# Optimization experiments

Hardware: AMD Instinct MI355X
Metric: run time of the kernel (lower is better)

The kernel has to match this reference:

```python
import jax, jax.numpy as jnp
import numpy as np

D_MODEL, D_STATE, D_CONV, EXPAND = 1024, 16, 4, 2
D_INNER = EXPAND * D_MODEL            # 2048
DT_RANK = int(np.ceil(D_MODEL / 16))  # 64
B, L = 2, 2048


def _dt_bias(key):
    # matches torch init: dt ~ exp(U(log dt_min, log dt_max)), inv via softplus inverse
    dt = jnp.exp(jax.random.uniform(key, (D_INNER,)) * (np.log(0.1) - np.log(0.001)) + np.log(0.001))
    dt = jnp.clip(dt, 1e-4, None)
    return dt + jnp.log(-jnp.expm1(-dt))


def _A_log():
    return jnp.log(jnp.tile(jnp.arange(1, D_STATE + 1, dtype=jnp.float32)[None, :], (D_INNER, 1)))


def setup_inputs() -> dict:
    key = jax.random.key(0)
    ks = jax.random.split(key, 16)
    n = lambda k, shape, s=0.02: jax.random.normal(k, shape, jnp.float32) * s
    return {
        "hidden_states": jax.random.normal(ks[0], (B, L, D_MODEL), jnp.float32),
        "in_proj_w": n(ks[1], (2 * D_INNER, D_MODEL)),
        "conv_w": n(ks[2], (D_INNER, 1, D_CONV), 0.2),
        "conv_b": jnp.zeros((D_INNER,), jnp.float32),
        "x_proj_w": n(ks[3], (DT_RANK + 2 * D_STATE, D_INNER)),
        "dt_proj_w": n(ks[4], (D_INNER, DT_RANK), 0.1),
        "dt_proj_b": _dt_bias(ks[5]),
        "A_log": _A_log(),
        "D": jnp.ones((D_INNER,), jnp.float32),
        "conv_w_b": n(ks[6], (D_INNER, 1, D_CONV), 0.2),
        "conv_b_b": jnp.zeros((D_INNER,), jnp.float32),
        "x_proj_w_b": n(ks[7], (DT_RANK + 2 * D_STATE, D_INNER)),
        "dt_proj_w_b": n(ks[8], (D_INNER, DT_RANK), 0.1),
        "dt_proj_b_b": _dt_bias(ks[9]),
        "A_b_log": _A_log(),
        "D_b": jnp.ones((D_INNER,), jnp.float32),
        "out_proj_w": n(ks[10], (D_MODEL, D_INNER)),
    }


def _silu(x):
    return x * jax.nn.sigmoid(x)


def _causal_dw_conv(x, w, b):
    # x: (B, Di, L); w: (Di, 1, K) depthwise; left-pad K-1 => causal, output length L
    y = jax.lax.conv_general_dilated(
        x, w, window_strides=(1,), padding=[(D_CONV - 1, 0)],
        dimension_numbers=("NCH", "OIH", "NCH"), feature_group_count=x.shape[1])
    return y + b[None, :, None]


def _mamba_branch(xz, conv_w, conv_b, x_proj_w, dt_proj_w, dt_proj_b, A_log, Dp):
    # xz: (B, 2*Di, L) -> y: (B, Di, L); selective scan (mamba_inner_fn_no_out_proj)
    x, z = jnp.split(xz, 2, axis=1)
    x = _silu(_causal_dw_conv(x, conv_w, conv_b))                       # (B,Di,L)
    x_dbl = jnp.einsum('rd,bdl->brl', x_proj_w, x)
    dt_r, Bc, Cc = jnp.split(x_dbl, [DT_RANK, DT_RANK + D_STATE], axis=1)
    delta = jax.nn.softplus(jnp.einsum('dr,brl->bdl', dt_proj_w, dt_r) + dt_proj_b[None, :, None])
    A = -jnp.exp(A_log)                                                 # (Di,N)

    def step(h, inp):
        d_t, u_t, b_t, c_t = inp   # (B,Di),(B,Di),(B,N),(B,N)
        h = h * jnp.exp(d_t[..., None] * A) + (d_t * u_t)[..., None] * b_t[:, None, :]
        return h, jnp.einsum('bdn,bn->bd', h, c_t)

    h0 = jnp.zeros((x.shape[0], D_INNER, D_STATE), x.dtype)
    xs = (jnp.moveaxis(delta, 2, 0), jnp.moveaxis(x, 2, 0),
          jnp.moveaxis(Bc, 2, 0), jnp.moveaxis(Cc, 2, 0))
    _, ys = jax.lax.scan(step, h0, xs)                                  # (L,B,Di)
    y = jnp.moveaxis(ys, 0, 2) + x * Dp[None, :, None]
    return y * _silu(z)


def reference(hidden_states, in_proj_w, conv_w, conv_b, x_proj_w, dt_proj_w, dt_proj_b,
              A_log, D, conv_w_b, conv_b_b, x_proj_w_b, dt_proj_w_b, dt_proj_b_b,
              A_b_log, D_b, out_proj_w):
    # bimamba_type == 'v2': forward scan + flipped backward scan, summed, then out_proj (no biases)
    xz = jnp.einsum('ed,bld->bel', in_proj_w, hidden_states)            # (B, 2*Di, L)
    out_f = _mamba_branch(xz, conv_w, conv_b, x_proj_w, dt_proj_w, dt_proj_b, A_log, D)
    out_r = _mamba_branch(xz[..., ::-1], conv_w_b, conv_b_b, x_proj_w_b,
                          dt_proj_w_b, dt_proj_b_b, A_b_log, D_b)[..., ::-1]
    y = out_f + out_r                                                   # (B,Di,L)
    return jnp.einsum('me,bel->blm', out_proj_w, y)                     # (B,L,D)
```

## Files before the change

kernel.cpp:

```cpp
#include <hip/hip_runtime.h>
#include <hip/hip_bf16.h>
#include <math.h>


#define L_SEQ  2048
#define B_SZ   2
#define DM     1024
#define DI     2048
#define NST    16
#define RTOT   96
#define DTR    64
#define NTOT   (B_SZ * L_SEQ)
#define ETOT   (2 * DI)
#define NCH    32
#define CHT    (L_SEQ / NCH)
#define SPLK   8

#define OFF_X    ((size_t)0)
#define OFF_ZT   (OFF_X   + (size_t)DI * NTOT)
#define OFF_XCF  (OFF_ZT  + (size_t)DI * NTOT)
#define OFF_XCB  (OFF_XCF + (size_t)DI * NTOT)
#define OFF_DLTB (OFF_XCB + (size_t)DI * NTOT)
#define OFF_XDF  (OFF_DLTB + (size_t)DI * NTOT)
#define OFF_XDB  (OFF_XDF + (size_t)RTOT * NTOT)
#define OFF_SS   (OFF_XDB + (size_t)RTOT * NTOT)
#define OFF_HL   (OFF_SS  + (size_t)4 * NCH * DI)
#define OFF_YGTF (OFF_HL  + (size_t)4 * NCH * NST * DI)
#define OFF_YGTB (OFF_YGTF + (size_t)NTOT * DI / 2)
#define OFF_XDT16F (OFF_YGTB + (size_t)NTOT * DI / 2)
#define OFF_XDT16B (OFF_XDT16F + (size_t)NTOT * DTR / 2)
#define OFF_DTW16F (OFF_XDT16B + (size_t)NTOT * DTR / 2)
#define OFF_DTW16B (OFF_DTW16F + (size_t)DI * DTR / 2)
#define WS_FLOATS  (OFF_DTW16B + (size_t)DI * DTR / 2)

typedef __bf16 bf16x8 __attribute__((ext_vector_type(8)));
typedef float  floatx4 __attribute__((ext_vector_type(4)));

__device__ __forceinline__ float silu_f(float x) {
    return x / (1.f + __expf(-x));
}

__device__ __forceinline__ void gl2lds16(const __bf16* g, __bf16* l) {
    __builtin_amdgcn_global_load_lds(
        (const __attribute__((address_space(1))) unsigned int*)g,
        (__attribute__((address_space(3))) unsigned int*)l, 16, 0, 0);
}

template<int MT, bool TRANS, bool SPLITZ>
__global__ __launch_bounds__(256)
void gemm_bf16(const __bf16* __restrict__ A, const __bf16* __restrict__ B,
               float* __restrict__ C, float* __restrict__ C2,
               int M, int N, int K)
{
    static_assert(MT == 64 || MT == 128, "vmcnt literals assume MT in {64,128}");
    __shared__ __attribute__((aligned(16))) __bf16 As[2][MT * 32];
    __shared__ __attribute__((aligned(16))) __bf16 Bs[2][128 * 32];
    const int tid  = threadIdx.x;
    const int m0   = blockIdx.y * MT;
    const int n0   = blockIdx.x * 128;
    const int lane = tid & 63;
    const int wave = tid >> 6;
    const int wy   = wave >> 1, wx = wave & 1;
    const int lr   = lane & 15;
    const int q    = lane >> 4;
    constexpr int MF = MT / 32;

    floatx4 acc[MF][4];
#pragma unroll
    for (int i = 0; i < MF; ++i)
#pragma unroll
        for (int j = 0; j < 4; ++j) acc[i][j] = (floatx4)(0.0f);

    const int rl = lane >> 2;
    const int cp = lane & 3;
    const int sw = (q ^ ((lr >> 2) & 3)) * 8;

    auto stage = [&](int s, int k0) {
#pragma unroll
        for (int is = 0; is < MT / 64; ++is) {
            int r0  = wave * (MT / 4) + is * 16;
            int row = r0 + rl;
            int c   = cp ^ ((row >> 2) & 3);
            gl2lds16(A + (size_t)(m0 + row) * K + k0 + c * 8, &As[s][r0 * 32]);
        }
#pragma unroll
        for (int is = 0; is < 2; ++is) {
            int r0  = wave * 32 + is * 16;
            int row = r0 + rl;
            int c   = cp ^ ((row >> 2) & 3);
            gl2lds16(B + (size_t)(n0 + row) * K + k0 + c * 8, &Bs[s][r0 * 32]);
        }
    };

    stage(0, 0);
    int cur = 0;
    for (int k0 = 0; k0 < K; k0 += 32) {
        if (k0 + 32 < K) {
            stage(cur ^ 1, k0 + 32);
            if constexpr (MT == 128) {
                asm volatile("s_waitcnt vmcnt(4)" ::: "memory");
            } else {
                asm volatile("s_waitcnt vmcnt(3)" ::: "memory");
            }
        } else {
            asm volatile("s_waitcnt vmcnt(0)" ::: "memory");
        }
        __builtin_amdgcn_s_barrier();

        bf16x8 af[MF], bfr[4];
#pragma unroll
        for (int i = 0; i < MF; ++i)
            af[i] = *(const bf16x8*)&As[cur][(wy * (MT / 2) + i * 16 + lr) * 32 + sw];
#pragma unroll
        for (int j = 0; j < 4; ++j)
            bfr[j] = *(const bf16x8*)&Bs[cur][(wx * 64 + j * 16 + lr) * 32 + sw];
#pragma unroll
        for (int i = 0; i < MF; ++i)
#pragma unroll
            for (int j = 0; j < 4; ++j)
                acc[i][j] = __builtin_amdgcn_mfma_f32_16x16x32_bf16(
                    af[i], bfr[j], acc[i][j], 0, 0, 0);
        __builtin_amdgcn_s_barrier();
        cur ^= 1;
    }

    const int mb = m0 + wy * (MT / 2);
    const int nb = n0 + wx * 64;
#pragma unroll
    for (int i = 0; i < MF; ++i) {
#pragma unroll
        for (int j = 0; j < 4; ++j) {
            int gn  = nb + j * 16 + lr;
            int gm0 = mb + i * 16 + q * 4;
            if constexpr (SPLITZ) {
                if (m0 < DI) {
#pragma unroll
                    for (int r = 0; r < 4; ++r)
                        C[(size_t)(gm0 + r) * N + gn] = acc[i][j][r];
                } else {
                    *(floatx4*)&C2[(size_t)gn * DI + (gm0 - DI)] = acc[i][j];
                }
            } else if constexpr (TRANS) {
                *(floatx4*)&C[(size_t)gn * M + gm0] = acc[i][j];
            } else {
#pragma unroll
                for (int r = 0; r < 4; ++r)
                    C[(size_t)(gm0 + r) * N + gn] = acc[i][j][r];
            }
        }
    }
}

__global__ __launch_bounds__(256)
void dtproj_mfma(const __bf16* __restrict__ Af, const __bf16* __restrict__ Ab,
                 const __bf16* __restrict__ Bwf, const __bf16* __restrict__ Bwb,
                 const float* __restrict__ bif, const float* __restrict__ bib,
                 float* __restrict__ outf, float* __restrict__ outb)
{
    __shared__ __attribute__((aligned(16))) __bf16 As[2][128 * 32];
    __shared__ __attribute__((aligned(16))) __bf16 Bs[2][128 * 32];
    const int br = blockIdx.z;
    const __bf16* A  = br ? Ab : Af;
    const __bf16* B  = br ? Bwb : Bwf;
    const float*  bi = br ? bib : bif;
    float*        C  = br ? outb : outf;

    const int tid  = threadIdx.x;
    const int m0   = blockIdx.y * 128;
    const int n0   = blockIdx.x * 128;
    const int lane = tid & 63;
    const int wave = tid >> 6;
    const int wy   = wave >> 1, wx = wave & 1;
    const int lr   = lane & 15;
    const int q    = lane >> 4;

    floatx4 acc[4][4];
#pragma unroll
    for (int i = 0; i < 4; ++i)
#pragma unroll
        for (int j = 0; j < 4; ++j) acc[i][j] = (floatx4)(0.0f);

    const int rl = lane >> 2;
    const int cp = lane & 3;
    const int sw = (q ^ ((lr >> 2) & 3)) * 8;

#pragma unroll
    for (int t = 0; t < 2; ++t) {
        int k0 = t * 32;
#pragma unroll
        for (int is = 0; is < 2; ++is) {
            int r0  = wave * 32 + is * 16;
            int row = r0 + rl;
            int c   = cp ^ ((row >> 2) & 3);
            gl2lds16(A + (size_t)(m0 + row) * DTR + k0 + c * 8, &As[t][r0 * 32]);
            gl2lds16(B + (size_t)(n0 + row) * DTR + k0 + c * 8, &Bs[t][r0 * 32]);
        }
    }

#pragma unroll
    for (int t = 0; t < 2; ++t) {
        if (t == 0) asm volatile("s_waitcnt vmcnt(4)" ::: "memory");
        else        asm volatile("s_waitcnt vmcnt(0)" ::: "memory");
        __builtin_amdgcn_s_barrier();

        bf16x8 af[4], bfr[4];
#pragma unroll
        for (int i = 0; i < 4; ++i)
            af[i] = *(const bf16x8*)&As[t][(wy * 64 + i * 16 + lr) * 32 + sw];
#pragma unroll
        for (int j = 0; j < 4; ++j)
            bfr[j] = *(const bf16x8*)&Bs[t][(wx * 64 + j * 16 + lr) * 32 + sw];
#pragma unroll
        for (int i = 0; i < 4; ++i)
#pragma unroll
            for (int j = 0; j < 4; ++j)
                acc[i][j] = __builtin_amdgcn_mfma_f32_16x16x32_bf16(
                    af[i], bfr[j], acc[i][j], 0, 0, 0);
    }

    const int mb = m0 + wy * 64;
    const int nb = n0 + wx * 64;
    float bj[4];
#pragma unroll
    for (int j = 0; j < 4; ++j) bj[j] = bi[nb + j * 16 + lr];
#pragma unroll
    for (int i = 0; i < 4; ++i) {
#pragma unroll
        for (int r = 0; r < 4; ++r) {
            int gm = mb + i * 16 + q * 4 + r;
#pragma unroll
            for (int j = 0; j < 4; ++j) {
                int gn = nb + j * 16 + lr;
                float x = acc[i][j][r] + bj[j];
                float o = (x > 20.f) ? x : __logf(1.f + __expf(x));
                C[(size_t)gm * DI + gn] = o;
            }
        }
    }
}

__global__ __launch_bounds__(256)
void cvt_bf16_k(const float* __restrict__ in, __bf16* __restrict__ out)
{
    const size_t i = ((size_t)blockIdx.x * 256 + threadIdx.x) * 8;
    float4 a = *(const float4*)(in + i);
    float4 b = *(const float4*)(in + i + 4);
    bf16x8 p;
    p[0]=(__bf16)a.x; p[1]=(__bf16)a.y; p[2]=(__bf16)a.z; p[3]=(__bf16)a.w;
    p[4]=(__bf16)b.x; p[5]=(__bf16)b.y; p[6]=(__bf16)b.z; p[7]=(__bf16)b.w;
    *(bf16x8*)(out + i) = p;
}

__global__ __launch_bounds__(256)
void addbf16_k(const __bf16* __restrict__ a, const __bf16* __restrict__ b,
               __bf16* __restrict__ o)
{
    const size_t i = ((size_t)blockIdx.x * 256 + threadIdx.x) * 8;
    bf16x8 x = *(const bf16x8*)(a + i);
    bf16x8 y = *(const bf16x8*)(b + i);
    bf16x8 s;
#pragma unroll
    for (int e = 0; e < 8; ++e) s[e] = (__bf16)((float)x[e] + (float)y[e]);
    *(bf16x8*)(o + i) = s;
}

__global__ __launch_bounds__(256)
void gemm_k3(const float* __restrict__ A, const float* __restrict__ Bm,
             float* __restrict__ C, int M, int N, int K)
{
    __shared__ float As[16][132];
    __shared__ float Bs[16][132];
    const int tid = threadIdx.x;
    const int n0 = blockIdx.x * 128;
    const int m0 = blockIdx.y * 128;
    int ksz  = K / (int)gridDim.z;
    int kbeg = blockIdx.z * ksz;
    int kend = kbeg + ksz;
    C += (size_t)blockIdx.z * M * N;
    const int tx = tid & 15, ty = tid >> 4;

    float acc[8][8];
#pragma unroll
    for (int i = 0; i < 8; ++i)
#pragma unroll
        for (int j = 0; j < 8; ++j) acc[i][j] = 0.f;

    for (int k0 = kbeg; k0 < kend; k0 += 16) {
#pragma unroll
        for (int it = 0; it < 2; ++it) {
            int i = tid + it * 256;
            int m = i >> 2, kq = i & 3;
            float4 v = make_float4(0.f, 0.f, 0.f, 0.f);
            int gm = m0 + m;
            if (gm < M) v = *(const float4*)(A + (size_t)gm * K + (k0 + kq * 4));
            As[kq * 4 + 0][m] = v.x; As[kq * 4 + 1][m] = v.y;
            As[kq * 4 + 2][m] = v.z; As[kq * 4 + 3][m] = v.w;
        }
#pragma unroll
        for (int it = 0; it < 2; ++it) {
            int i = tid + it * 256;
            int n = i >> 2, kq = i & 3;
            float4 v = *(const float4*)(Bm + (size_t)(n0 + n) * K + (k0 + kq * 4));
            Bs[kq * 4 + 0][n] = v.x; Bs[kq * 4 + 1][n] = v.y;
            Bs[kq * 4 + 2][n] = v.z; Bs[kq * 4 + 3][n] = v.w;
        }
        __syncthreads();
#pragma unroll
        for (int kk = 0; kk < 16; ++kk) {
            float av[8], bv[8];
            *(float4*)&av[0] = *(const float4*)&As[kk][ty * 8];
            *(float4*)&av[4] = *(const float4*)&As[kk][ty * 8 + 4];
            *(float4*)&bv[0] = *(const float4*)&Bs[kk][tx * 8];
            *(float4*)&bv[4] = *(const float4*)&Bs[kk][tx * 8 + 4];
#pragma unroll
            for (int i = 0; i < 8; ++i)
#pragma unroll
                for (int j = 0; j < 8; ++j)
                    acc[i][j] = fmaf(av[i], bv[j], acc[i][j]);
        }
        __syncthreads();
    }

#pragma unroll
    for (int i = 0; i < 8; ++i) {
        int gm = m0 + ty * 8 + i;
        if (gm < M) {
            float* cp = C + (size_t)gm * N + n0 + tx * 8;
            *(float4*)cp       = make_float4(acc[i][0], acc[i][1], acc[i][2], acc[i][3]);
            *(float4*)(cp + 4) = make_float4(acc[i][4], acc[i][5], acc[i][6], acc[i][7]);
        }
    }
}

__global__ __launch_bounds__(256)
void reduce8t_k(const float* __restrict__ P, float* __restrict__ out,
                __bf16* __restrict__ out2, size_t stride)
{
    const size_t i4 = ((size_t)blockIdx.x * 256 + threadIdx.x) * 4;
    float4 s = *(const float4*)(P + i4);
#pragma unroll
    for (int z = 1; z < SPLK; ++z) {
        float4 v = *(const float4*)(P + (size_t)z * stride + i4);
        s.x += v.x; s.y += v.y; s.z += v.z; s.w += v.w;
    }
    *(float4*)(out + i4) = s;
    const int r = (int)(i4 >> 12);
    if (r < DTR) {
        const int n = (int)(i4 & (NTOT - 1));
        out2[(size_t)(n + 0) * DTR + r] = (__bf16)s.x;
        out2[(size_t)(n + 1) * DTR + r] = (__bf16)s.y;
        out2[(size_t)(n + 2) * DTR + r] = (__bf16)s.z;
        out2[(size_t)(n + 3) * DTR + r] = (__bf16)s.w;
    }
}

__global__ __launch_bounds__(256)
void conv_k(const float* __restrict__ x,
            const float* __restrict__ wf, const float* __restrict__ bf,
            const float* __restrict__ wb, const float* __restrict__ bb,
            float* __restrict__ xcf, float* __restrict__ xcb)
{
    __shared__ float xs[70 * 65];
    const int tid = threadIdx.x;
    const int d0 = blockIdx.x * 64;
    const int n0 = blockIdx.y * 64;
    const int b  = n0 >> 11;
    const int l0 = n0 & (L_SEQ - 1);
    const size_t bbase = (size_t)b << 11;

    for (int i = tid; i < 64 * 70; i += 256) {
        int r = i / 70, c = i % 70;
        int l = l0 - 3 + c;
        float v = 0.f;
        if (l >= 0 && l < L_SEQ) v = x[(size_t)(d0 + r) * NTOT + bbase + l];
        xs[c * 65 + r] = v;
    }
    __syncthreads();

    const int dd = tid & 63;
    const int lq = tid >> 6;
    const int d  = d0 + dd;
    const float w0 = wf[d * 4 + 0], w1 = wf[d * 4 + 1];
    const float w2 = wf[d * 4 + 2], w3 = wf[d * 4 + 3];
    const float v0 = wb[d * 4 + 0], v1 = wb[d * 4 + 1];
    const float v2 = wb[d * 4 + 2], v3 = wb[d * 4 + 3];
    const float bfv = bf[d], bbv = bb[d];

    for (int lr = 0; lr < 64; lr += 4) {
        const int lo = lr + lq;
        const int l  = l0 + lo;
        float x0 = xs[(lo + 0) * 65 + dd];
        float x1 = xs[(lo + 1) * 65 + dd];
        float x2 = xs[(lo + 2) * 65 + dd];
        float x3 = xs[(lo + 3) * 65 + dd];
        float x4 = xs[(lo + 4) * 65 + dd];
        float x5 = xs[(lo + 5) * 65 + dd];
        float x6 = xs[(lo + 6) * 65 + dd];
        float xf = bfv + w0 * x0 + w1 * x1 + w2 * x2 + w3 * x3;
        xcf[((size_t)bbase + l) * DI + d] = silu_f(xf);
        float xb = bbv + v3 * x3 + v2 * x4 + v1 * x5 + v0 * x6;
        xcb[((size_t)bbase + (L_SEQ - 1 - l)) * DI + d] = silu_f(xb);
    }
}

__global__ __launch_bounds__(256)
void scan_part1(const float* __restrict__ xcf, const float* __restrict__ xcb,
                const float* __restrict__ xdf, const float* __restrict__ xdb,
                const float* __restrict__ dltf, const float* __restrict__ dltb,
                const float* __restrict__ Alog_f, const float* __restrict__ Alog_b,
                float* __restrict__ SS, float* __restrict__ HL)
{
    __shared__ float Bsh[NST][CHT];
    const int tid = threadIdx.x;
    const int d  = blockIdx.x * 256 + tid;
    const int c  = blockIdx.y;
    const int bb = blockIdx.z;
    const int b  = bb & 1;
    const int br = bb >> 1;

    const float* u    = br ? xcb : xcf;
    const float* dl   = br ? dltb : dltf;
    const float* xd   = br ? xdb : xdf;
    const float* Alog = br ? Alog_b : Alog_f;

    const size_t nbase = (size_t)b * L_SEQ + (size_t)c * CHT;
    const float* bcB = xd + (size_t)DTR * NTOT + nbase;

    for (int i = tid; i < NST * CHT; i += 256) {
        int n = i >> 6;
        int t = i & (CHT - 1);
        Bsh[n][t] = bcB[(size_t)n * NTOT + t];
    }

    float Arow[NST], h[NST];
#pragma unroll
    for (int n = 0; n < NST; ++n) {
        Arow[n] = -__expf(Alog[d * NST + n]);
        h[n] = 0.f;
    }
    float S = 0.f;

    const float* up = u  + nbase * DI + d;
    const float* dp = dl + nbase * DI + d;

    __syncthreads();

    float dv[4], uv[4];
#pragma unroll
    for (int k = 0; k < 4; ++k) {
        dv[k] = dp[(size_t)k * DI];
        uv[k] = up[(size_t)k * DI];
    }

    for (int tr = 0; tr < CHT; tr += 4) {
        float dvn[4], uvn[4];
#pragma unroll
        for (int k = 0; k < 4; ++k) {
            dvn[k] = dp[(size_t)(tr + 4 + k) * DI];
            uvn[k] = up[(size_t)(tr + 4 + k) * DI];
        }
        S += (dv[0] + dv[1]) + (dv[2] + dv[3]);
        float du[4] = { dv[0]*uv[0], dv[1]*uv[1], dv[2]*uv[2], dv[3]*uv[3] };
#pragma unroll
        for (int n = 0; n < NST; ++n) {
            float4 Bn = *(const float4*)&Bsh[n][tr];
            float hn = h[n];
            float An = Arow[n];
            hn = hn * __expf(dv[0] * An) + du[0] * Bn.x;
            hn = hn * __expf(dv[1] * An) + du[1] * Bn.y;
            hn = hn * __expf(dv[2] * An) + du[2] * Bn.z;
            hn = hn * __expf(dv[3] * An) + du[3] * Bn.w;
            h[n] = hn;
        }
#pragma unroll
        for (int k = 0; k < 4; ++k) { dv[k] = dvn[k]; uv[k] = uvn[k]; }
    }
    SS[((size_t)bb * NCH + c) * DI + d] = S;
#pragma unroll
    for (int n = 0; n < NST; ++n)
        HL[(((size_t)bb * NCH + c) * NST + n) * DI + d] = h[n];
}

__global__ __launch_bounds__(256)
void scan_part2(const float* __restrict__ SS, float* HL,
                const float* __restrict__ Alog_f, const float* __restrict__ Alog_b)
{
    const int d  = blockIdx.x * 256 + threadIdx.x;
    const int n  = blockIdx.y;
    const int bb = blockIdx.z;
    const int br = bb >> 1;
    const float* Alog = br ? Alog_b : Alog_f;
    const float A = -__expf(Alog[d * NST + n]);

    float H = 0.f;
#pragma unroll
    for (int c = 0; c < NCH; ++c) {
        const size_t si = ((size_t)bb * NCH + c) * DI + d;
        const size_t hi = (((size_t)bb * NCH + c) * NST + n) * DI + d;
        float hl = HL[hi];
        HL[hi] = H;
        H = __expf(SS[si] * A) * H + hl;
    }
}

__global__ __launch_bounds__(256)
void scan_part3(const float* __restrict__ zt,
                const float* __restrict__ xcf, const float* __restrict__ xcb,
                const float* __restrict__ xdf, const float* __restrict__ xdb,
                const float* __restrict__ dltf, const float* __restrict__ dltb,
                const float* __restrict__ HIN,
                __bf16* __restrict__ ygtf, __bf16* __restrict__ ygtb,
                const float* __restrict__ Alog_f, const float* __restrict__ Alog_b,
                const float* __restrict__ Df, const float* __restrict__ Db)
{
    __shared__ float BCs[2 * NST][CHT];
    const int tid = threadIdx.x;
    const int d  = blockIdx.x * 256 + tid;
    const int c  = blockIdx.y;
    const int bb = blockIdx.z;
    const int b  = bb & 1;
    const int br = bb >> 1;

    const float* u    = br ? xcb : xcf;
    const float* dl   = br ? dltb : dltf;
    const float* xd   = br ? xdb : xdf;
    const float* Alog = br ? Alog_b : Alog_f;
    const float* Dv   = br ? Db : Df;
    __bf16*      ygt  = br ? ygtb : ygtf;

    const size_t nbase = (size_t)b * L_SEQ + (size_t)c * CHT;
    const float* bcB = xd + (size_t)DTR * NTOT + nbase;

    for (int i = tid; i < 2 * NST * CHT; i += 256) {
        int n = i >> 6;
        int t = i & (CHT - 1);
        BCs[n][t] = bcB[(size_t)n * NTOT + t];
    }

    float Arow[NST], h[NST];
#pragma unroll
    for (int n = 0; n < NST; ++n) {
        Arow[n] = -__expf(Alog[d * NST + n]);
        h[n] = HIN[(((size_t)bb * NCH + c) * NST + n) * DI + d];
    }
    const float Dp = Dv[d];

    const float* up = u  + nbase * DI + d;
    const float* dp = dl + nbase * DI + d;
    const size_t bL = (size_t)b * L_SEQ;
    const int    t0 = c * CHT;

    __syncthreads();

    float dv[4], uv[4];
#pragma unroll
    for (int k = 0; k < 4; ++k) {
        dv[k] = dp[(size_t)k * DI];
        uv[k] = up[(size_t)k * DI];
    }

    for (int tr = 0; tr < CHT; tr += 4) {
        float dvn[4], uvn[4];
#pragma unroll
        for (int k = 0; k < 4; ++k) {
            dvn[k] = dp[(size_t)(tr + 4 + k) * DI];
            uvn[k] = up[(size_t)(tr + 4 + k) * DI];
        }
        size_t nn[4];
        float  zv[4];
#pragma unroll
        for (int k = 0; k < 4; ++k) {
            int t = t0 + tr + k;
            nn[k] = br ? (bL + (L_SEQ - 1 - t)) : (bL + t);
            zv[k] = zt[nn[k] * DI + d];
        }
        float du[4] = { dv[0]*uv[0], dv[1]*uv[1], dv[2]*uv[2], dv[3]*uv[3] };
        float y[4] = { 0.f, 0.f, 0.f, 0.f };
#pragma unroll
        for (int n = 0; n < NST; ++n) {
            float4 Bn = *(const float4*)&BCs[n][tr];
            float4 Cn = *(const float4*)&BCs[NST + n][tr];
            float hn = h[n];
            float An = Arow[n];
            hn = hn * __expf(dv[0] * An) + du[0] * Bn.x;  y[0] = fmaf(hn, Cn.x, y[0]);
            hn = hn * __expf(dv[1] * An) + du[1] * Bn.y;  y[1] = fmaf(hn, Cn.y, y[1]);
            hn = hn * __expf(dv[2] * An) + du[2] * Bn.z;  y[2] = fmaf(hn, Cn.z, y[2]);
            hn = hn * __expf(dv[3] * An) + du[3] * Bn.w;  y[3] = fmaf(hn, Cn.w, y[3]);
            h[n] = hn;
        }
#pragma unroll
        for (int k = 0; k < 4; ++k) {
            float yo = (y[k] + uv[k] * Dp) * silu_f(zv[k]);
            ygt[nn[k] * DI + d] = (__bf16)yo;
        }
#pragma unroll
        for (int k = 0; k < 4; ++k) { dv[k] = dvn[k]; uv[k] = uvn[k]; }
    }
}

extern "C" void kernel_launch(void* const* d_in, const int* in_sizes, int n_in,
                              void* d_out, int out_size, void* d_ws, size_t ws_size,
                              hipStream_t stream)
{
    const float* hid     = (const float*)d_in[0];
    const float* inw     = (const float*)d_in[1];
    const float* convw   = (const float*)d_in[2];
    const float* convb   = (const float*)d_in[3];
    const float* xpw     = (const float*)d_in[4];
    const float* dtw     = (const float*)d_in[5];
    const float* dtb     = (const float*)d_in[6];
    const float* Alog    = (const float*)d_in[7];
    const float* Dv      = (const float*)d_in[8];
    const float* convw_b = (const float*)d_in[9];
    const float* convb_b = (const float*)d_in[10];
    const float* xpw_b   = (const float*)d_in[11];
    const float* dtw_b   = (const float*)d_in[12];
    const float* dtb_b   = (const float*)d_in[13];
    const float* Alog_b  = (const float*)d_in[14];
    const float* Dv_b    = (const float*)d_in[15];
    const float* outw    = (const float*)d_in[16];
    float* out = (float*)d_out;
    float* ws  = (float*)d_ws;

    if (ws_size < WS_FLOATS * sizeof(float)) return;

    float*  X    = ws + OFF_X;
    float*  ZT   = ws + OFF_ZT;
    float*  XCF  = ws + OFF_XCF;
    float*  XCB  = ws + OFF_XCB;
    float*  DLTB = ws + OFF_DLTB;
    float*  XDF  = ws + OFF_XDF;
    float*  XDB  = ws + OFF_XDB;
    float*  SS   = ws + OFF_SS;
    float*  HLb  = ws + OFF_HL;
    __bf16* YGTF = (__bf16*)(ws + OFF_YGTF);
    __bf16* YGTB = (__bf16*)(ws + OFF_YGTB);
    float*  PF   = ws + OFF_YGTF;
    float*  PB   = ws + OFF_YGTB;
    float*  DLTF = X;
    __bf16* IW16 = (__bf16*)(ws + OFF_SS);
    __bf16* HD16 = IW16 + (size_t)ETOT * DM;
    __bf16* OW16 = (__bf16*)(ws + OFF_XCB);
    __bf16* YGS  = (__bf16*)(ws + OFF_XCF);
    __bf16* XDT16F = (__bf16*)(ws + OFF_XDT16F);
    __bf16* XDT16B = (__bf16*)(ws + OFF_XDT16B);
    __bf16* DTW16F = (__bf16*)(ws + OFF_DTW16F);
    __bf16* DTW16B = (__bf16*)(ws + OFF_DTW16B);

    dim3 blk(256);
    cvt_bf16_k<<<dim3(ETOT * DM / 2048), blk, 0, stream>>>(inw, IW16);
    cvt_bf16_k<<<dim3(NTOT * DM / 2048), blk, 0, stream>>>(hid, HD16);
    cvt_bf16_k<<<dim3(DI * DTR / 2048), blk, 0, stream>>>(dtw, DTW16F);
    cvt_bf16_k<<<dim3(DI * DTR / 2048), blk, 0, stream>>>(dtw_b, DTW16B);
    gemm_bf16<128, false, true><<<dim3(32, 32), blk, 0, stream>>>(
        IW16, HD16, X, ZT, ETOT, NTOT, DM);
    conv_k<<<dim3(32, 64), blk, 0, stream>>>(X, convw, convb, convw_b, convb_b, XCF, XCB);
    gemm_k3<<<dim3(32, 1, SPLK), blk, 0, stream>>>(xpw, XCF, PF, RTOT, NTOT, DI);
    gemm_k3<<<dim3(32, 1, SPLK), blk, 0, stream>>>(xpw_b, XCB, PB, RTOT, NTOT, DI);
    reduce8t_k<<<dim3(RTOT * NTOT / 1024), blk, 0, stream>>>(PF, XDF, XDT16F, (size_t)RTOT * NTOT);
    reduce8t_k<<<dim3(RTOT * NTOT / 1024), blk, 0, stream>>>(PB, XDB, XDT16B, (size_t)RTOT * NTOT);
    dtproj_mfma<<<dim3(DI / 128, NTOT / 128, 2), blk, 0, stream>>>(
        XDT16F, XDT16B, DTW16F, DTW16B, dtb, dtb_b, DLTF, DLTB);
    scan_part1<<<dim3(DI / 256, NCH, 4), blk, 0, stream>>>(
        XCF, XCB, XDF, XDB, DLTF, DLTB, Alog, Alog_b, SS, HLb);
    scan_part2<<<dim3(DI / 256, NST, 4), blk, 0, stream>>>(
        SS, HLb, Alog, Alog_b);
    scan_part3<<<dim3(DI / 256, NCH, 4), blk, 0, stream>>>(
        ZT, XCF, XCB, XDF, XDB, DLTF, DLTB, HLb, YGTF, YGTB, Alog, Alog_b, Dv, Dv_b);
    cvt_bf16_k<<<dim3(DM * DI / 2048), blk, 0, stream>>>(outw, OW16);
    addbf16_k<<<dim3(NTOT * DI / 2048), blk, 0, stream>>>(YGTF, YGTB, YGS);
    gemm_bf16<64, true, false><<<dim3(32, 16), blk, 0, stream>>>(
        OW16, YGS, out, nullptr, DM, NTOT, DI);

    (void)in_sizes; (void)n_in; (void)out_size;
}
```

Baseline: 482.0 us.

## Split scan state dimension across four lanes per channel in chunked scan

scan_part1 and scan_part3 now assign each channel to four threads, each owning four of the sixteen SSM states, and launch four times as many blocks. In part3 the per-state output contributions are combined with a 4-lane xor shuffle reduction, and each lane writes one timestep of the group of four. The shared B/C buffers are padded to reduce bank conflicts. This raises thread-level parallelism and cuts per-thread registers, at the cost of each lane redundantly loading delta and u and doing extra shuffles.

New measurement: 505.8 us. +4.9%, slower.

```diff
diff --git a/kernel.cpp b/kernel.cpp
--- a/kernel.cpp
+++ b/kernel.cpp
@@ -14,6 +14,7 @@
 #define ETOT   (2 * DI)
 #define NCH    32
 #define CHT    (L_SEQ / NCH)
+#define CHP    (CHT + 4)
 #define SPLK   8
 
 #define OFF_X    ((size_t)0)
@@ -410,16 +411,18 @@
                 const float* __restrict__ Alog_f, const float* __restrict__ Alog_b,
                 float* __restrict__ SS, float* __restrict__ HL)
 {
-    __shared__ float Bsh[NST][CHT];
+    __shared__ float Bsh[NST][CHP];
     const int tid = threadIdx.x;
-    const int d  = blockIdx.x * 256 + tid;
-    const int c  = blockIdx.y;
-    const int bb = blockIdx.z;
-    const int b  = bb & 1;
-    const int br = bb >> 1;
+    const int sg  = tid & 3;
+    const int dl  = tid >> 2;
+    const int d   = blockIdx.x * 64 + dl;
+    const int c   = blockIdx.y;
+    const int bb  = blockIdx.z;
+    const int b   = bb & 1;
+    const int br  = bb >> 1;
 
     const float* u    = br ? xcb : xcf;
-    const float* dl   = br ? dltb : dltf;
+    const float* dl_  = br ? dltb : dltf;
     const float* xd   = br ? xdb : xdf;
     const float* Alog = br ? Alog_b : Alog_f;
 
@@ -432,16 +435,17 @@
         Bsh[n][t] = bcB[(size_t)n * NTOT + t];
     }
 
-    float Arow[NST], h[NST];
-#pragma unroll
-    for (int n = 0; n < NST; ++n) {
-        Arow[n] = -__expf(Alog[d * NST + n]);
-        h[n] = 0.f;
+    float Arow[4], h[4];
+    float4 a4 = *(const float4*)&Alog[(size_t)d * NST + sg * 4];
+#pragma unroll
+    for (int j = 0; j < 4; ++j) {
+        Arow[j] = -__expf(((const float*)&a4)[j]);
+        h[j] = 0.f;
     }
     float S = 0.f;
 
-    const float* up = u  + nbase * DI + d;
-    const float* dp = dl + nbase * DI + d;
+    const float* up = u   + nbase * DI + d;
+    const float* dp = dl_ + nbase * DI + d;
 
     __syncthreads();
 
@@ -462,23 +466,23 @@
         S += (dv[0] + dv[1]) + (dv[2] + dv[3]);
         float du[4] = { dv[0]*uv[0], dv[1]*uv[1], dv[2]*uv[2], dv[3]*uv[3] };
 #pragma unroll
-        for (int n = 0; n < NST; ++n) {
-            float4 Bn = *(const float4*)&Bsh[n][tr];
-            float hn = h[n];
-            float An = Arow[n];
+        for (int j = 0; j < 4; ++j) {
+            float4 Bn = *(const float4*)&Bsh[sg * 4 + j][tr];
+            float hn = h[j];
+            float An = Arow[j];
             hn = hn * __expf(dv[0] * An) + du[0] * Bn.x;
             hn = hn * __expf(dv[1] * An) + du[1] * Bn.y;
             hn = hn * __expf(dv[2] * An) + du[2] * Bn.z;
             hn = hn * __expf(dv[3] * An) + du[3] * Bn.w;
-            h[n] = hn;
+            h[j] = hn;
         }
 #pragma unroll
         for (int k = 0; k < 4; ++k) { dv[k] = dvn[k]; uv[k] = uvn[k]; }
     }
-    SS[((size_t)bb * NCH + c) * DI + d] = S;
-#pragma unroll
-    for (int n = 0; n < NST; ++n)
-        HL[(((size_t)bb * NCH + c) * NST + n) * DI + d] = h[n];
+    if (sg == 0) SS[((size_t)bb * NCH + c) * DI + d] = S;
+#pragma unroll
+    for (int j = 0; j < 4; ++j)
+        HL[(((size_t)bb * NCH + c) * NST + sg * 4 + j) * DI + d] = h[j];
 }
 
 __global__ __launch_bounds__(256)
@@ -513,16 +517,18 @@
                 const float* __restrict__ Alog_f, const float* __restrict__ Alog_b,
                 const float* __restrict__ Df, const float* __restrict__ Db)
 {
-    __shared__ float BCs[2 * NST][CHT];
+    __shared__ float BCs[2 * NST][CHP];
     const int tid = threadIdx.x;
-    const int d  = blockIdx.x * 256 + tid;
-    const int c  = blockIdx.y;
-    const int bb = blockIdx.z;
-    const int b  = bb & 1;
-    const int br = bb >> 1;
+    const int sg  = tid & 3;
+    const int dl  = tid >> 2;
+    const int d   = blockIdx.x * 64 + dl;
+    const int c   = blockIdx.y;
+    const int bb  = blockIdx.z;
+    const int b   = bb & 1;
+    const int br  = bb >> 1;
 
     const float* u    = br ? xcb : xcf;
-    const float* dl   = br ? dltb : dltf;
+    const float* dl_  = br ? dltb : dltf;
     const float* xd   = br ? xdb : xdf;
     const float* Alog = br ? Alog_b : Alog_f;
     const float* Dv   = br ? Db : Df;
@@ -537,16 +543,17 @@
         BCs[n][t] = bcB[(size_t)n * NTOT + t];
     }
 
-    float Arow[NST], h[NST];
-#pragma unroll
-    for (int n = 0; n < NST; ++n) {
-        Arow[n] = -__expf(Alog[d * NST + n]);
-        h[n] = HIN[(((size_t)bb * NCH + c) * NST + n) * DI + d];
+    float Arow[4], h[4];
+    float4 a4 = *(const float4*)&Alog[(size_t)d * NST + sg * 4];
+#pragma unroll
+    for (int j = 0; j < 4; ++j) {
+        Arow[j] = -__expf(((const float*)&a4)[j]);
+        h[j] = HIN[(((size_t)bb * NCH + c) * NST + sg * 4 + j) * DI + d];
     }
     const float Dp = Dv[d];
 
-    const float* up = u  + nbase * DI + d;
-    const float* dp = dl + nbase * DI + d;
+    const float* up = u   + nbase * DI + d;
+    const float* dp = dl_ + nbase * DI + d;
     const size_t bL = (size_t)b * L_SEQ;
     const int    t0 = c * CHT;
 
@@ -566,33 +573,33 @@
             dvn[k] = dp[(size_t)(tr + 4 + k) * DI];
             uvn[k] = up[(size_t)(tr + 4 + k) * DI];
         }
-        size_t nn[4];
-        float  zv[4];
-#pragma unroll
-        for (int k = 0; k < 4; ++k) {
-            int t = t0 + tr + k;
-            nn[k] = br ? (bL + (L_SEQ - 1 - t)) : (bL + t);
-            zv[k] = zt[nn[k] * DI + d];
-        }
+        const int tk = t0 + tr + sg;
+        const size_t nnk = br ? (bL + (L_SEQ - 1 - tk)) : (bL + tk);
+        const float zvk = zt[nnk * DI + d];
+
         float du[4] = { dv[0]*uv[0], dv[1]*uv[1], dv[2]*uv[2], dv[3]*uv[3] };
         float y[4] = { 0.f, 0.f, 0.f, 0.f };
 #pragma unroll
-        for (int n = 0; n < NST; ++n) {
-            float4 Bn = *(const float4*)&BCs[n][tr];
-            float4 Cn = *(const float4*)&BCs[NST + n][tr];
-            float hn = h[n];
-            float An = Arow[n];
+        for (int j = 0; j < 4; ++j) {
+            float4 Bn = *(const float4*)&BCs[sg * 4 + j][tr];
+            float4 Cn = *(const float4*)&BCs[NST + sg * 4 + j][tr];
+            float hn = h[j];
+            float An = Arow[j];
             hn = hn * __expf(dv[0] * An) + du[0] * Bn.x;  y[0] = fmaf(hn, Cn.x, y[0]);
             hn = hn * __expf(dv[1] * An) + du[1] * Bn.y;  y[1] = fmaf(hn, Cn.y, y[1]);
             hn = hn * __expf(dv[2] * An) + du[2] * Bn.z;  y[2] = fmaf(hn, Cn.z, y[2]);
             hn = hn * __expf(dv[3] * An) + du[3] * Bn.w;  y[3] = fmaf(hn, Cn.w, y[3]);
-            h[n] = hn;
+            h[j] = hn;
         }
 #pragma unroll
         for (int k = 0; k < 4; ++k) {
-            float yo = (y[k] + uv[k] * Dp) * silu_f(zv[k]);
-            ygt[nn[k] * DI + d] = (__bf16)yo;
-        }
+            y[k] += __shfl_xor(y[k], 1, 4);
+            y[k] += __shfl_xor(y[k], 2, 4);
+        }
+        float ysel = (sg == 0) ? y[0] : (sg == 1) ? y[1] : (sg == 2) ? y[2] : y[3];
+        float usel = (sg == 0) ? uv[0] : (sg == 1) ? uv[1] : (sg == 2) ? uv[2] : uv[3];
+        float yo = (ysel + usel * Dp) * silu_f(zvk);
+        ygt[nnk * DI + d] = (__bf16)yo;
 #pragma unroll
         for (int k = 0; k < 4; ++k) { dv[k] = dvn[k]; uv[k] = uvn[k]; }
     }
@@ -661,11 +668,11 @@
     reduce8t_k<<<dim3(RTOT * NTOT / 1024), blk, 0, stream>>>(PB, XDB, XDT16B, (size_t)RTOT * NTOT);
     dtproj_mfma<<<dim3(DI / 128, NTOT / 128, 2), blk, 0, stream>>>(
         XDT16F, XDT16B, DTW16F, DTW16B, dtb, dtb_b, DLTF, DLTB);
-    scan_part1<<<dim3(DI / 256, NCH, 4), blk, 0, stream>>>(
+    scan_part1<<<dim3(DI / 64, NCH, 4), blk, 0, stream>>>(
         XCF, XCB, XDF, XDB, DLTF, DLTB, Alog, Alog_b, SS, HLb);
     scan_part2<<<dim3(DI / 256, NST, 4), blk, 0, stream>>>(
         SS, HLb, Alog, Alog_b);
-    scan_part3<<<dim3(DI / 256, NCH, 4), blk, 0, stream>>>(
+    scan_part3<<<dim3(DI / 64, NCH, 4), blk, 0, stream>>>(
         ZT, XCF, XCB, XDF, XDB, DLTF, DLTB, HLb, YGTF, YGTB, Alog, Alog_b, Dv, Dv_b);
     cvt_bf16_k<<<dim3(DM * DI / 2048), blk, 0, stream>>>(outw, OW16);
     addbf16_k<<<dim3(NTOT * DI / 2048), blk, 0, stream>>>(YGTF, YGTB, YGS);
```
